# Kernel optimization log

Hardware: AMD Instinct MI355X
Metric: run time of the kernel (lower is better)

Reference implementation:

```python
import jax, jax.numpy as jnp
import numpy as np

EPS = 0.1
MAX_ITER = 10
SIGMA = 0.1
NEG_INF = -1e8


def gaussian_position_filter(in_size, out_size, dtype):
    a = jnp.arange(0.0, in_size, dtype=dtype)[:, None] / in_size
    b = jnp.arange(0.0, out_size, dtype=dtype)[None, :] / out_size
    return jnp.exp(-(((a - b) / SIGMA) ** 2))[None]


def log_sinkhorn(K, mask, max_iter):
    # K: n x in_size x out_size (already scaled by 1/eps); mask: n x in_size bool
    n, in_size, out_size = K.shape
    dt = K.dtype
    loga = jnp.log((out_size / mask.sum(1, keepdims=True)).astype(dt))  # n x 1

    def neg_lse(u, v, axis):
        Z = K + u[:, :, None] + v[:, None, :]
        return -jax.nn.logsumexp(Z, axis=axis)

    def body(carry, _):
        u, v = carry
        u = loga + neg_lse(u, v, -1)           # row update: n x in_size
        u = jnp.where(mask, u, jnp.asarray(NEG_INF, dt))
        v = neg_lse(u, v, 1)                   # col update: n x out_size
        return (u, v), None

    u0 = jnp.zeros((n, in_size), dt)
    v0 = jnp.zeros((n, out_size), dt)
    (u, v), _ = jax.lax.scan(body, (u0, v0), None, length=max_iter)
    return jnp.exp(K + u[:, :, None] + v[:, None, :])  # transport plan T


def setup_inputs() -> dict:
    key = jax.random.key(0)
    k1, k2, k3 = jax.random.split(key, 3)
    B, S, O, D = 16, 4096, 512, 128
    return {
        "input": jax.random.normal(k1, (B, S, D), jnp.float32),
        "target": jax.random.normal(k2, (B, O, D), jnp.float32),
        "iou_cost": jax.random.uniform(k3, (B, S, O), jnp.float32),
        "mask": jnp.ones((B, S), jnp.bool_),
    }


def reference(input, target, iou_cost, mask):
    # input: B x S x D, target: B x O x D, iou_cost: B x S x O, mask: B x S
    B, S, D = input.shape
    O = target.shape[1]
    pf = gaussian_position_filter(S, O, input.dtype)
    K = jnp.einsum('bsd,bod->bso', input, target) - iou_cost  # similarity minus IoU cost
    K = pf * K / EPS
    T = pf * log_sinkhorn(K, mask, MAX_ITER) * S              # B x S x O
    # output: B x (out_size*heads) x in_size, heads=1
    return jnp.transpose(T, (0, 2, 1)).reshape(B, O, S)
```

## Files before the change

### kernel.cpp

```cpp
#include <hip/hip_runtime.h>
#include <hip/hip_bf16.h>

#define B_ 16
#define S_ 4096
#define O_ 512
#define D_ 128
#define NEG_INF_ -1e8f
#define MAX_ITER_ 10
#define YST 513

typedef __attribute__((ext_vector_type(8))) short short8;
typedef __attribute__((ext_vector_type(4))) float floatx4;
typedef __attribute__((ext_vector_type(4))) unsigned short ushort4v;

__device__ inline unsigned short f32_to_bf16_rne(float x) {
    union { float f; unsigned int u; } c; c.f = x;
    unsigned int u = c.u;
    unsigned int r = (u + 0x7FFFu + ((u >> 16) & 1u)) >> 16;
    return (unsigned short)r;
}
__device__ inline float bf16_bits_to_f32(unsigned short h) {
    union { unsigned int u; float f; } c; c.u = ((unsigned int)h) << 16;
    return c.f;
}

__global__ void init_kernel(const int* __restrict__ mask,
                            float* __restrict__ u, float* __restrict__ v,
                            float* __restrict__ loga) {
    __shared__ int sc[256];
    int b = blockIdx.x, t = threadIdx.x;
    int c = 0;
    for (int k = t; k < S_; k += 256) c += (mask[(size_t)b * S_ + k] != 0);
    sc[t] = c; __syncthreads();
    for (int st = 128; st > 0; st >>= 1) { if (t < st) sc[t] += sc[t + st]; __syncthreads(); }
    if (t == 0) loga[b] = logf((float)O_ / (float)sc[0]);
    for (int k = t; k < S_; k += 256) u[(size_t)b * S_ + k] = 0.f;
    for (int k = t; k < O_; k += 256) v[b * O_ + k] = 0.f;
}

__global__ __launch_bounds__(256) void split_kernel(const float* __restrict__ src,
                                                    unsigned short* __restrict__ hi,
                                                    unsigned short* __restrict__ lo, int n4) {
    int i = blockIdx.x * 256 + threadIdx.x;
    if (i >= n4) return;
    float4 x = ((const float4*)src)[i];
    float xs[4] = {x.x, x.y, x.z, x.w};
    ushort4v h, l;
#pragma unroll
    for (int j = 0; j < 4; ++j) {
        unsigned short hh = f32_to_bf16_rne(xs[j]);
        float rem = xs[j] - bf16_bits_to_f32(hh);
        h[j] = hh; l[j] = f32_to_bf16_rne(rem);
    }
    ((ushort4v*)hi)[i] = h;
    ((ushort4v*)lo)[i] = l;
}


__global__ __launch_bounds__(256) void gemm_nat(const unsigned short* __restrict__ in_hi,
                                                const unsigned short* __restrict__ in_lo,
                                                const unsigned short* __restrict__ tg_hi,
                                                const unsigned short* __restrict__ tg_lo,
                                                const float* __restrict__ iou,
                                                float* __restrict__ K) {
    int b = blockIdx.z;
    int s0 = blockIdx.x * 256;
    int o0 = blockIdx.y * 64;
    int t = threadIdx.x, wid = t >> 6, lane = t & 63, fr = lane & 15, kg = lane >> 4;
    int sw = s0 + wid * 64;

    const unsigned short* ih = in_hi + ((size_t)b * S_ + sw + fr) * D_;
    const unsigned short* il = in_lo + ((size_t)b * S_ + sw + fr) * D_;
    const unsigned short* th = tg_hi + ((size_t)b * O_ + o0 + fr) * D_;
    const unsigned short* tl = tg_lo + ((size_t)b * O_ + o0 + fr) * D_;

    floatx4 acc[4][4];
#pragma unroll
    for (int i = 0; i < 4; ++i)
#pragma unroll
        for (int j = 0; j < 4; ++j) acc[i][j] = (floatx4){0.f, 0.f, 0.f, 0.f};

#pragma unroll
    for (int kb = 0; kb < 4; ++kb) {
        int ko = kb * 32 + kg * 8;
        short8 T_h[4], T_l[4];
#pragma unroll
        for (int j = 0; j < 4; ++j) {
            T_h[j] = *(const short8*)(th + (size_t)j * 16 * D_ + ko);
            T_l[j] = *(const short8*)(tl + (size_t)j * 16 * D_ + ko);
        }
#pragma unroll
        for (int i = 0; i < 4; ++i) {
            short8 I_h = *(const short8*)(ih + (size_t)i * 16 * D_ + ko);
            short8 I_l = *(const short8*)(il + (size_t)i * 16 * D_ + ko);
#pragma unroll
            for (int j = 0; j < 4; ++j) {
                acc[i][j] = __builtin_amdgcn_mfma_f32_16x16x32_bf16(T_l[j], I_h, acc[i][j], 0, 0, 0);
                acc[i][j] = __builtin_amdgcn_mfma_f32_16x16x32_bf16(T_h[j], I_l, acc[i][j], 0, 0, 0);
                acc[i][j] = __builtin_amdgcn_mfma_f32_16x16x32_bf16(T_h[j], I_h, acc[i][j], 0, 0, 0);
            }
        }
    }

#pragma unroll
    for (int i = 0; i < 4; ++i) {
        int s = sw + i * 16 + fr;
        float sn = (float)s * (1.0f / S_);
        size_t rowb = ((size_t)b * S_ + s) * O_;
#pragma unroll
        for (int j = 0; j < 4; ++j) {
            int ob = o0 + j * 16 + kg * 4;
            float4 iv = *(const float4*)(iou + rowb + ob);
            float ivs[4] = {iv.x, iv.y, iv.z, iv.w};
            float tmp[4];
#pragma unroll
            for (int r = 0; r < 4; ++r) {
                float d = sn - (float)(ob + r) * (1.0f / O_);
                float pf = __expf(-100.0f * d * d);
                tmp[r] = pf * (acc[i][j][r] - ivs[r]) * 10.0f;
            }
            float4 q; q.x = tmp[0]; q.y = tmp[1]; q.z = tmp[2]; q.w = tmp[3];
            *(float4*)(K + rowb + ob) = q;
        }
    }
}

template <int FIRST>
__global__ __launch_bounds__(256) void sink_iter(const float* __restrict__ K,
                                                 const float* __restrict__ vin,
                                                 float* __restrict__ u,
                                                 float2* __restrict__ colma,
                                                 const int* __restrict__ mask,
                                                 const float* __restrict__ loga) {
    __shared__ float sv[O_];
    __shared__ float sy[16 * YST];
    int b = blockIdx.y;
    int t = threadIdx.x;
    int fr = t & 15, sl = t >> 4;
    if (!FIRST) {
        for (int i = t; i < O_; i += 256) sv[i] = vin[b * O_ + i];
        __syncthreads();
    }
    int s = blockIdx.x * 16 + sl;
    size_t srow = (size_t)b * S_ + s;
    const float* krow = K + srow * O_ + fr * 4;
    float uold = FIRST ? 0.f : u[srow];

    float xv[32];
#pragma unroll
    for (int k = 0; k < 8; ++k) {
        float4 q = *(const float4*)(krow + k * 64);
        if (!FIRST) {
            float4 vv = *(const float4*)&sv[fr * 4 + k * 64];
            q.x += uold + vv.x; q.y += uold + vv.y;
            q.z += uold + vv.z; q.w += uold + vv.w;
        }
        xv[k * 4 + 0] = q.x; xv[k * 4 + 1] = q.y;
        xv[k * 4 + 2] = q.z; xv[k * 4 + 3] = q.w;
    }

    float M = -INFINITY;
#pragma unroll
    for (int i = 0; i < 32; ++i) M = fmaxf(M, xv[i]);
#pragma unroll
    for (int off = 1; off < 16; off <<= 1) M = fmaxf(M, __shfl_xor(M, off));
    float a = 0.f;
#pragma unroll
    for (int i = 0; i < 32; ++i) a += __expf(xv[i] - M);
#pragma unroll
    for (int off = 1; off < 16; off <<= 1) a += __shfl_xor(a, off);
    float unew = loga[b] - (M + logf(a));
    if (!mask[srow]) unew = NEG_INF_;
    if (fr == 0) u[srow] = unew;

    float c = unew - uold;
#pragma unroll
    for (int k = 0; k < 8; ++k) {
        float4 q;
        q.x = xv[k * 4 + 0] + c; q.y = xv[k * 4 + 1] + c;
        q.z = xv[k * 4 + 2] + c; q.w = xv[k * 4 + 3] + c;
        *(float4*)&sy[sl * YST + fr * 4 + k * 64] = q;
    }
    __syncthreads();

    float2* cout = colma + ((size_t)b * 256 + blockIdx.x) * O_;
#pragma unroll
    for (int h = 0; h < 2; ++h) {
        int o = t + h * 256;
        float q[16];
        float m = -INFINITY;
#pragma unroll
        for (int r = 0; r < 16; ++r) { q[r] = sy[r * YST + o]; m = fmaxf(m, q[r]); }
        float aa = 0.f;
#pragma unroll
        for (int r = 0; r < 16; ++r) aa += __expf(q[r] - m);
        float2 res; res.x = m; res.y = aa;
        cout[o] = res;
    }
}

__global__ __launch_bounds__(256) void finalize_v(const float2* __restrict__ colma,
                                                  float* __restrict__ v) {
    __shared__ float sm[4][64], sa[4][64];
    int b = blockIdx.y;
    int ol = threadIdx.x & 63, cg = threadIdx.x >> 6;
    int o = blockIdx.x * 64 + ol;
    const float2* cp = colma + (size_t)b * 256 * O_ + o;
    float M = -INFINITY, A = 0.f;
#pragma unroll 4
    for (int i = 0; i < 64; ++i) {
        float2 q = cp[(size_t)(cg * 64 + i) * O_];
        float nm = fmaxf(M, q.x);
        A = A * __expf(M - nm) + q.y * __expf(q.x - nm);
        M = nm;
    }
    sm[cg][ol] = M; sa[cg][ol] = A;
    __syncthreads();
    if (threadIdx.x < 64) {
        M = sm[0][ol]; A = sa[0][ol];
#pragma unroll
        for (int i = 1; i < 4; ++i) {
            float mi = sm[i][ol], ai = sa[i][ol];
            float nm = fmaxf(M, mi);
            A = A * __expf(M - nm) + ai * __expf(mi - nm);
            M = nm;
        }
        v[b * O_ + o] = -(M + logf(A));
    }
}

__global__ __launch_bounds__(256) void final_tr(const float* __restrict__ K,
                                                const float* __restrict__ u,
                                                const float* __restrict__ v,
                                                float* __restrict__ out) {
    __shared__ float tile[64][65];
    __shared__ float su[64], svv[64];
    int b = blockIdx.z;
    int s0 = blockIdx.x * 64, o0 = blockIdx.y * 64;
    int t = threadIdx.x, fr = t & 15, rg = t >> 4;
    if (t < 64) su[t] = u[(size_t)b * S_ + s0 + t];
    else if (t < 128) svv[t - 64] = v[b * O_ + o0 + t - 64];
    __syncthreads();
#pragma unroll
    for (int p = 0; p < 4; ++p) {
        int sl = p * 16 + rg;
        int s = s0 + sl;
        float4 x = *(const float4*)(K + ((size_t)b * S_ + s) * O_ + o0 + fr * 4);
        float us = su[sl];
        float sn = (float)s * (1.0f / S_);
        float xs[4] = {x.x, x.y, x.z, x.w};
#pragma unroll
        for (int c = 0; c < 4; ++c) {
            int ol = fr * 4 + c;
            float d = sn - (float)(o0 + ol) * (1.0f / O_);
            tile[ol][sl] = 4096.0f * __expf(xs[c] + us + svv[ol] - 100.0f * d * d);
        }
    }
    __syncthreads();
#pragma unroll
    for (int p = 0; p < 4; ++p) {
        int ol = p * 16 + rg;
        float4 y;
        y.x = tile[ol][fr * 4 + 0];
        y.y = tile[ol][fr * 4 + 1];
        y.z = tile[ol][fr * 4 + 2];
        y.w = tile[ol][fr * 4 + 3];
        *(float4*)(out + ((size_t)b * O_ + o0 + ol) * S_ + s0 + fr * 4) = y;
    }
}


__global__ __launch_bounds__(256) void gemm_kt2(const unsigned short* __restrict__ in_hi,
                                                const unsigned short* __restrict__ in_lo,
                                                const unsigned short* __restrict__ tg_hi,
                                                const unsigned short* __restrict__ tg_lo,
                                                const float* __restrict__ iou,
                                                float* __restrict__ KT) {
    __shared__ float siou[64 * 65];
    int b = blockIdx.z;
    int s0 = blockIdx.x * 64;
    int o0 = blockIdx.y * 64;
    int t = threadIdx.x;
    {
        const float* ir = iou + ((size_t)b * S_ + s0 + (t >> 2)) * O_ + o0 + (t & 3) * 16;
        float4 q0 = ((const float4*)ir)[0];
        float4 q1 = ((const float4*)ir)[1];
        float4 q2 = ((const float4*)ir)[2];
        float4 q3 = ((const float4*)ir)[3];
        float* dst = &siou[(t >> 2) * 65 + (t & 3) * 16];
        dst[0]=q0.x; dst[1]=q0.y; dst[2]=q0.z; dst[3]=q0.w;
        dst[4]=q1.x; dst[5]=q1.y; dst[6]=q1.z; dst[7]=q1.w;
        dst[8]=q2.x; dst[9]=q2.y; dst[10]=q2.z; dst[11]=q2.w;
        dst[12]=q3.x; dst[13]=q3.y; dst[14]=q3.z; dst[15]=q3.w;
    }
    int w = t >> 6, lane = t & 63, fr = lane & 15, kg = lane >> 4;
    const unsigned short* ta_hi = tg_hi + ((size_t)b * O_ + o0 + w * 16 + fr) * D_;
    const unsigned short* ta_lo = tg_lo + ((size_t)b * O_ + o0 + w * 16 + fr) * D_;
    const unsigned short* ib_hi = in_hi + ((size_t)b * S_ + s0 + fr) * D_;
    const unsigned short* ib_lo = in_lo + ((size_t)b * S_ + s0 + fr) * D_;
    floatx4 acc[4];
#pragma unroll
    for (int st = 0; st < 4; ++st) acc[st] = (floatx4){0.f, 0.f, 0.f, 0.f};
#pragma unroll
    for (int kb = 0; kb < 4; ++kb) {
        int ko = kb * 32 + kg * 8;
        short8 ah = *(const short8*)(ta_hi + ko);
        short8 al2 = *(const short8*)(ta_lo + ko);
#pragma unroll
        for (int st = 0; st < 4; ++st) {
            short8 bh2 = *(const short8*)(ib_hi + (size_t)st * 16 * D_ + ko);
            short8 bl2 = *(const short8*)(ib_lo + (size_t)st * 16 * D_ + ko);
            acc[st] = __builtin_amdgcn_mfma_f32_16x16x32_bf16(al2, bh2, acc[st], 0, 0, 0);
            acc[st] = __builtin_amdgcn_mfma_f32_16x16x32_bf16(ah, bl2, acc[st], 0, 0, 0);
            acc[st] = __builtin_amdgcn_mfma_f32_16x16x32_bf16(ah, bh2, acc[st], 0, 0, 0);
        }
    }
    __syncthreads();
#pragma unroll
    for (int st = 0; st < 4; ++st) {
        int s = s0 + st * 16 + fr;
        float ds = (float)s * (1.0f / S_);
#pragma unroll
        for (int r = 0; r < 4; ++r) {
            int o = o0 + w * 16 + kg * 4 + r;
            float d = ds - (float)o * (1.0f / O_);
            float pf = __expf(-100.0f * d * d);
            float iouv = siou[(st * 16 + fr) * 65 + (w * 16 + kg * 4 + r)];
            KT[((size_t)b * O_ + o) * S_ + s] = pf * (acc[st][r] - iouv) * 10.0f;
        }
    }
}

__global__ __launch_bounds__(256) void row_update2(const float* __restrict__ KT,
                                                   const float* __restrict__ v,
                                                   float* __restrict__ u,
                                                   const int* __restrict__ mask,
                                                   const float* __restrict__ loga) {
    __shared__ float sv[O_];
    __shared__ float lm[4][128], la[4][128];
    int b = blockIdx.y;
    int s0 = blockIdx.x * 128;
    int t = threadIdx.x, lane = t & 63, w = t >> 6;
    for (int i = t; i < O_; i += 256) sv[i] = v[b * O_ + i];
    __syncthreads();
    const float* kt = KT + (size_t)b * O_ * S_ + s0 + lane * 2;
    float m0 = -INFINITY, m1 = -INFINITY, a0 = 0.f, a1 = 0.f;
    int ob = w * 128;
#pragma unroll 8
    for (int i = 0; i < 128; ++i) {
        int o = ob + i;
        float2 x2 = *(const float2*)(kt + (size_t)o * S_);
        float vo = sv[o];
        float x0 = x2.x + vo, x1 = x2.y + vo;
        if (x0 > m0) { a0 = a0 * __expf(m0 - x0) + 1.f; m0 = x0; } else a0 += __expf(x0 - m0);
        if (x1 > m1) { a1 = a1 * __expf(m1 - x1) + 1.f; m1 = x1; } else a1 += __expf(x1 - m1);
    }
    lm[w][lane * 2] = m0;     la[w][lane * 2] = a0;
    lm[w][lane * 2 + 1] = m1; la[w][lane * 2 + 1] = a1;
    __syncthreads();
    if (t < 128) {
        float M = lm[0][t], A = la[0][t];
#pragma unroll
        for (int i = 1; i < 4; ++i) {
            float mi = lm[i][t], ai = la[i][t];
            float nm = fmaxf(M, mi);
            A = A * __expf(M - nm) + ai * __expf(mi - nm);
            M = nm;
        }
        float lse = M + logf(A);
        size_t si = (size_t)b * S_ + s0 + t;
        u[si] = mask[si] ? (loga[b] - u[si] - lse) : NEG_INF_;
    }
}

template <int FIN>
__global__ __launch_bounds__(256) void col_update2(float* __restrict__ KT,
                                                   const float* __restrict__ u,
                                                   float* __restrict__ v) {
    __shared__ float red[8];
    int b = blockIdx.y, o = blockIdx.x;
    int t = threadIdx.x;
    float* kt = KT + ((size_t)b * O_ + o) * S_;
    const float* ub = u + (size_t)b * S_;
    float vold = v[b * O_ + o];
    float xs[16];
    float m = -INFINITY, a = 0.f;
#pragma unroll
    for (int k = 0; k < 4; ++k) {
        int s = k * 1024 + t * 4;
        float4 kx = *(const float4*)(kt + s);
        float4 ux = *(const float4*)(ub + s);
        float x0 = kx.x + ux.x, x1 = kx.y + ux.y, x2 = kx.z + ux.z, x3 = kx.w + ux.w;
        if (FIN) { xs[k*4] = x0; xs[k*4+1] = x1; xs[k*4+2] = x2; xs[k*4+3] = x3; }
        float cm = fmaxf(fmaxf(x0, x1), fmaxf(x2, x3));
        float nm = fmaxf(m, cm);
        a = a * __expf(m - nm) + __expf(x0 - nm) + __expf(x1 - nm)
                               + __expf(x2 - nm) + __expf(x3 - nm);
        m = nm;
    }
#pragma unroll
    for (int off = 1; off < 64; off <<= 1) {
        float mo = __shfl_xor(m, off), ao = __shfl_xor(a, off);
        float nm = fmaxf(m, mo);
        a = a * __expf(m - nm) + ao * __expf(mo - nm);
        m = nm;
    }
    int w = t >> 6;
    if ((t & 63) == 0) { red[w * 2] = m; red[w * 2 + 1] = a; }
    __syncthreads();
    float M = red[0], A = red[1];
#pragma unroll
    for (int i = 1; i < 4; ++i) {
        float mi = red[i * 2], ai = red[i * 2 + 1];
        float nm = fmaxf(M, mi);
        A = A * __expf(M - nm) + ai * __expf(mi - nm);
        M = nm;
    }
    float lse = M + logf(A);
    float vn = -vold - lse;
    if (t == 0) v[b * O_ + o] = vn;
    if (FIN) {
        float oo = (float)o * (1.0f / O_);
#pragma unroll
        for (int k = 0; k < 4; ++k) {
            int s = k * 1024 + t * 4;
            float4 r;
            float rr[4];
#pragma unroll
            for (int j = 0; j < 4; ++j) {
                float d = (float)(s + j) * (1.0f / S_) - oo;
                rr[j] = 4096.0f * __expf(xs[k * 4 + j] + vn - 100.0f * d * d);
            }
            r.x = rr[0]; r.y = rr[1]; r.z = rr[2]; r.w = rr[3];
            *(float4*)(kt + s) = r;
        }
    }
}


extern "C" void kernel_launch(void* const* d_in, const int* in_sizes, int n_in,
                              void* d_out, int out_size, void* d_ws, size_t ws_size,
                              hipStream_t stream) {
    const float* input  = (const float*)d_in[0];
    const float* target = (const float*)d_in[1];
    const float* iou    = (const float*)d_in[2];
    const int*   mask   = (const int*)d_in[3];
    float* out = (float*)d_out;
    float* wsf = (float*)d_ws;

    const size_t N_IN = (size_t)B_ * S_ * D_;
    const size_t N_TG = (size_t)B_ * O_ * D_;
    const size_t NK   = (size_t)B_ * S_ * O_;

    float* u    = wsf;
    float* v    = u + (size_t)B_ * S_;
    float* loga = v + (size_t)B_ * O_;

    float* Knat = loga + 16;
    float* region = Knat + NK;
    unsigned short* f_in_hi = (unsigned short*)region;
    unsigned short* f_in_lo = f_in_hi + N_IN;
    unsigned short* f_tg_hi = f_in_lo + N_IN;
    unsigned short* f_tg_lo = f_tg_hi + N_TG;
    float2* colma = (float2*)region;
    size_t need_fast = (size_t)((char*)(f_tg_lo + N_TG) - (char*)d_ws);

    unsigned short* m_in_hi = (unsigned short*)(loga + 16);
    unsigned short* m_in_lo = m_in_hi + N_IN;
    unsigned short* m_tg_hi = m_in_lo + N_IN;
    unsigned short* m_tg_lo = m_tg_hi + N_TG;
    size_t need_mid = (size_t)((char*)(m_tg_lo + N_TG) - (char*)d_ws);

    init_kernel<<<B_, 256, 0, stream>>>(mask, u, v, loga);

    if (ws_size >= need_fast) {
        split_kernel<<<(int)(N_IN / 4 / 256), 256, 0, stream>>>(input, f_in_hi, f_in_lo, (int)(N_IN / 4));
        split_kernel<<<(int)(N_TG / 4 / 256), 256, 0, stream>>>(target, f_tg_hi, f_tg_lo, (int)(N_TG / 4));
        gemm_nat<<<dim3(S_ / 256, O_ / 64, B_), 256, 0, stream>>>(f_in_hi, f_in_lo, f_tg_hi, f_tg_lo, iou, Knat);
        for (int it = 0; it < MAX_ITER_; ++it) {
            if (it == 0)
                sink_iter<1><<<dim3(S_ / 16, B_), 256, 0, stream>>>(Knat, v, u, colma, mask, loga);
            else
                sink_iter<0><<<dim3(S_ / 16, B_), 256, 0, stream>>>(Knat, v, u, colma, mask, loga);
            finalize_v<<<dim3(O_ / 64, B_), 256, 0, stream>>>(colma, v);
        }
        final_tr<<<dim3(S_ / 64, O_ / 64, B_), 256, 0, stream>>>(Knat, u, v, out);
    } else if (ws_size >= need_mid) {
        split_kernel<<<(int)(N_IN / 4 / 256), 256, 0, stream>>>(input, m_in_hi, m_in_lo, (int)(N_IN / 4));
        split_kernel<<<(int)(N_TG / 4 / 256), 256, 0, stream>>>(target, m_tg_hi, m_tg_lo, (int)(N_TG / 4));
        gemm_kt2<<<dim3(S_ / 64, O_ / 64, B_), 256, 0, stream>>>(m_in_hi, m_in_lo, m_tg_hi, m_tg_lo, iou, out);
        for (int it = 0; it < MAX_ITER_; ++it) {
            row_update2<<<dim3(S_ / 128, B_), 256, 0, stream>>>(out, v, u, mask, loga);
            if (it < MAX_ITER_ - 1)
                col_update2<0><<<dim3(O_, B_), 256, 0, stream>>>(out, u, v);
            else
                col_update2<1><<<dim3(O_, B_), 256, 0, stream>>>(out, u, v);
        }
    }
}
```

Baseline: 513.4 us.

## Prefetch IoU into LDS in GEMM and pipeline multi-tile sinkhorn row blocks

The GEMM now uses 128-row tiles and loads its IoU tile into shared memory with asynchronous global-to-LDS loads. The load uses a rotated column swizzle, so it overlaps the MFMA work and the epilogue reads avoid bank conflicts. Each sink_iter block now handles 64 rows as four 16-row sub-tiles, double-buffering the K loads in registers. Column max/sum partials are merged online across the sub-tiles, which shrinks the colma partial buffer and the finalize_v reduction fourfold. The trade-offs are higher register pressure, extra barriers, and fewer blocks per launch.

After: 518.7 us. Within noise of the previous version (+1.0%).

```diff
diff --git a/kernel.cpp b/kernel.cpp
--- a/kernel.cpp
+++ b/kernel.cpp
@@ -22,6 +22,10 @@
 __device__ inline float bf16_bits_to_f32(unsigned short h) {
     union { unsigned int u; float f; } c; c.u = ((unsigned int)h) << 16;
     return c.f;
+}
+__device__ inline void gload_lds16(const float* g, float* l) {
+    __builtin_amdgcn_global_load_lds((const __attribute__((address_space(1))) void*)g,
+                                     (__attribute__((address_space(3))) void*)l, 16, 0, 0);
 }
 
 __global__ void init_kernel(const int* __restrict__ mask,
@@ -56,27 +60,35 @@
     ((ushort4v*)lo)[i] = l;
 }
 
-
 __global__ __launch_bounds__(256) void gemm_nat(const unsigned short* __restrict__ in_hi,
                                                 const unsigned short* __restrict__ in_lo,
                                                 const unsigned short* __restrict__ tg_hi,
                                                 const unsigned short* __restrict__ tg_lo,
                                                 const float* __restrict__ iou,
                                                 float* __restrict__ K) {
+    __shared__ float siou[128 * 64];
     int b = blockIdx.z;
-    int s0 = blockIdx.x * 256;
+    int s0 = blockIdx.x * 128;
     int o0 = blockIdx.y * 64;
     int t = threadIdx.x, wid = t >> 6, lane = t & 63, fr = lane & 15, kg = lane >> 4;
-    int sw = s0 + wid * 64;
-
-    const unsigned short* ih = in_hi + ((size_t)b * S_ + sw + fr) * D_;
-    const unsigned short* il = in_lo + ((size_t)b * S_ + sw + fr) * D_;
+
+#pragma unroll
+    for (int i = 0; i < 8; ++i) {
+        int ii = wid * 8 + i;
+        int row = ii * 4 + (lane >> 4);
+        int col = (((lane & 15) + (row & 15)) & 15) * 4;
+        const float* g = iou + ((size_t)b * S_ + s0 + row) * O_ + o0 + col;
+        gload_lds16(g, &siou[ii * 256]);
+    }
+
+    const unsigned short* ih = in_hi + ((size_t)b * S_ + s0 + wid * 32 + fr) * D_;
+    const unsigned short* il = in_lo + ((size_t)b * S_ + s0 + wid * 32 + fr) * D_;
     const unsigned short* th = tg_hi + ((size_t)b * O_ + o0 + fr) * D_;
     const unsigned short* tl = tg_lo + ((size_t)b * O_ + o0 + fr) * D_;
 
-    floatx4 acc[4][4];
-#pragma unroll
-    for (int i = 0; i < 4; ++i)
+    floatx4 acc[2][4];
+#pragma unroll
+    for (int i = 0; i < 2; ++i)
 #pragma unroll
         for (int j = 0; j < 4; ++j) acc[i][j] = (floatx4){0.f, 0.f, 0.f, 0.f};
 
@@ -90,7 +102,7 @@
             T_l[j] = *(const short8*)(tl + (size_t)j * 16 * D_ + ko);
         }
 #pragma unroll
-        for (int i = 0; i < 4; ++i) {
+        for (int i = 0; i < 2; ++i) {
             short8 I_h = *(const short8*)(ih + (size_t)i * 16 * D_ + ko);
             short8 I_l = *(const short8*)(il + (size_t)i * 16 * D_ + ko);
 #pragma unroll
@@ -101,26 +113,29 @@
             }
         }
     }
-
-#pragma unroll
-    for (int i = 0; i < 4; ++i) {
-        int s = sw + i * 16 + fr;
+    __syncthreads();
+
+#pragma unroll
+    for (int i = 0; i < 2; ++i) {
+        int rowl = wid * 32 + i * 16 + fr;
+        int s = s0 + rowl;
         float sn = (float)s * (1.0f / S_);
         size_t rowb = ((size_t)b * S_ + s) * O_;
 #pragma unroll
         for (int j = 0; j < 4; ++j) {
-            int ob = o0 + j * 16 + kg * 4;
-            float4 iv = *(const float4*)(iou + rowb + ob);
+            int obl = j * 16 + kg * 4;
+            int x = (obl - fr * 4) & 63;
+            float4 iv = *(const float4*)&siou[rowl * 64 + x];
             float ivs[4] = {iv.x, iv.y, iv.z, iv.w};
             float tmp[4];
 #pragma unroll
             for (int r = 0; r < 4; ++r) {
-                float d = sn - (float)(ob + r) * (1.0f / O_);
+                float d = sn - (float)(o0 + obl + r) * (1.0f / O_);
                 float pf = __expf(-100.0f * d * d);
                 tmp[r] = pf * (acc[i][j][r] - ivs[r]) * 10.0f;
             }
             float4 q; q.x = tmp[0]; q.y = tmp[1]; q.z = tmp[2]; q.w = tmp[3];
-            *(float4*)(K + rowb + ob) = q;
+            *(float4*)(K + rowb + o0 + obl) = q;
         }
     }
 }
@@ -135,67 +150,98 @@
     __shared__ float sv[O_];
     __shared__ float sy[16 * YST];
     int b = blockIdx.y;
-    int t = threadIdx.x;
-    int fr = t & 15, sl = t >> 4;
+    int t = threadIdx.x, fr = t & 15, sl = t >> 4;
     if (!FIRST) {
         for (int i = t; i < O_; i += 256) sv[i] = vin[b * O_ + i];
         __syncthreads();
     }
-    int s = blockIdx.x * 16 + sl;
-    size_t srow = (size_t)b * S_ + s;
-    const float* krow = K + srow * O_ + fr * 4;
-    float uold = FIRST ? 0.f : u[srow];
-
-    float xv[32];
-#pragma unroll
-    for (int k = 0; k < 8; ++k) {
-        float4 q = *(const float4*)(krow + k * 64);
-        if (!FIRST) {
-            float4 vv = *(const float4*)&sv[fr * 4 + k * 64];
-            q.x += uold + vv.x; q.y += uold + vv.y;
-            q.z += uold + vv.z; q.w += uold + vv.w;
-        }
-        xv[k * 4 + 0] = q.x; xv[k * 4 + 1] = q.y;
-        xv[k * 4 + 2] = q.z; xv[k * 4 + 3] = q.w;
-    }
-
-    float M = -INFINITY;
-#pragma unroll
-    for (int i = 0; i < 32; ++i) M = fmaxf(M, xv[i]);
-#pragma unroll
-    for (int off = 1; off < 16; off <<= 1) M = fmaxf(M, __shfl_xor(M, off));
-    float a = 0.f;
-#pragma unroll
-    for (int i = 0; i < 32; ++i) a += __expf(xv[i] - M);
-#pragma unroll
-    for (int off = 1; off < 16; off <<= 1) a += __shfl_xor(a, off);
-    float unew = loga[b] - (M + logf(a));
-    if (!mask[srow]) unew = NEG_INF_;
-    if (fr == 0) u[srow] = unew;
-
-    float c = unew - uold;
-#pragma unroll
-    for (int k = 0; k < 8; ++k) {
-        float4 q;
-        q.x = xv[k * 4 + 0] + c; q.y = xv[k * 4 + 1] + c;
-        q.z = xv[k * 4 + 2] + c; q.w = xv[k * 4 + 3] + c;
-        *(float4*)&sy[sl * YST + fr * 4 + k * 64] = q;
-    }
-    __syncthreads();
-
-    float2* cout = colma + ((size_t)b * 256 + blockIdx.x) * O_;
-#pragma unroll
-    for (int h = 0; h < 2; ++h) {
-        int o = t + h * 256;
-        float q[16];
-        float m = -INFINITY;
-#pragma unroll
-        for (int r = 0; r < 16; ++r) { q[r] = sy[r * YST + o]; m = fmaxf(m, q[r]); }
-        float aa = 0.f;
-#pragma unroll
-        for (int r = 0; r < 16; ++r) aa += __expf(q[r] - m);
-        float2 res; res.x = m; res.y = aa;
-        cout[o] = res;
+    int sbase = blockIdx.x * 64;
+    float lg = loga[b];
+    float Mc0 = -INFINITY, Ac0 = 0.f, Mc1 = -INFINITY, Ac1 = 0.f;
+
+    float bufA[32], bufB[32];
+    auto loadK = [&](float (&dst)[32], int tau) {
+        const float* krow = K + ((size_t)b * S_ + sbase + tau * 16 + sl) * O_ + fr * 4;
+#pragma unroll
+        for (int k = 0; k < 8; ++k) {
+            float4 q = *(const float4*)(krow + k * 64);
+            dst[k * 4 + 0] = q.x; dst[k * 4 + 1] = q.y;
+            dst[k * 4 + 2] = q.z; dst[k * 4 + 3] = q.w;
+        }
+    };
+    auto process = [&](float (&cur)[32], float (&nxt)[32], int tau, bool pre) {
+        int s = sbase + tau * 16 + sl;
+        size_t srow = (size_t)b * S_ + s;
+        float uold = FIRST ? 0.f : u[srow];
+        int mk = mask[srow];
+        if (pre) loadK(nxt, tau + 1);
+
+        float xv[32];
+        if (FIRST) {
+#pragma unroll
+            for (int i = 0; i < 32; ++i) xv[i] = cur[i];
+        } else {
+#pragma unroll
+            for (int k = 0; k < 8; ++k) {
+                float4 vvq = *(const float4*)&sv[fr * 4 + k * 64];
+                xv[k * 4 + 0] = cur[k * 4 + 0] + uold + vvq.x;
+                xv[k * 4 + 1] = cur[k * 4 + 1] + uold + vvq.y;
+                xv[k * 4 + 2] = cur[k * 4 + 2] + uold + vvq.z;
+                xv[k * 4 + 3] = cur[k * 4 + 3] + uold + vvq.w;
+            }
+        }
+        float M = -INFINITY;
+#pragma unroll
+        for (int i = 0; i < 32; ++i) M = fmaxf(M, xv[i]);
+#pragma unroll
+        for (int off = 1; off < 16; off <<= 1) M = fmaxf(M, __shfl_xor(M, off));
+        float a = 0.f;
+#pragma unroll
+        for (int i = 0; i < 32; ++i) a += __expf(xv[i] - M);
+#pragma unroll
+        for (int off = 1; off < 16; off <<= 1) a += __shfl_xor(a, off);
+        float unew = lg - (M + logf(a));
+        if (!mk) unew = NEG_INF_;
+        if (fr == 0) u[srow] = unew;
+
+        float c = unew - uold;
+#pragma unroll
+        for (int k = 0; k < 8; ++k) {
+            float4 q;
+            q.x = xv[k * 4 + 0] + c; q.y = xv[k * 4 + 1] + c;
+            q.z = xv[k * 4 + 2] + c; q.w = xv[k * 4 + 3] + c;
+            *(float4*)&sy[sl * YST + fr * 4 + k * 64] = q;
+        }
+        __syncthreads();
+#pragma unroll
+        for (int h = 0; h < 2; ++h) {
+            int o = t + h * 256;
+            float q[16];
+            float m = -INFINITY;
+#pragma unroll
+            for (int r = 0; r < 16; ++r) { q[r] = sy[r * YST + o]; m = fmaxf(m, q[r]); }
+            float aa = 0.f;
+#pragma unroll
+            for (int r = 0; r < 16; ++r) aa += __expf(q[r] - m);
+            float Mo = h ? Mc1 : Mc0, Ao = h ? Ac1 : Ac0;
+            float nm = fmaxf(Mo, m);
+            Ao = Ao * __expf(Mo - nm) + aa * __expf(m - nm);
+            if (h) { Mc1 = nm; Ac1 = Ao; } else { Mc0 = nm; Ac0 = Ao; }
+        }
+        __syncthreads();
+    };
+    loadK(bufA, 0);
+    process(bufA, bufB, 0, true);
+    process(bufB, bufA, 1, true);
+    process(bufA, bufB, 2, true);
+    process(bufB, bufA, 3, false);
+
+    float2* cout = colma + ((size_t)b * 64 + blockIdx.x) * O_;
+    {
+        float2 r0; r0.x = Mc0; r0.y = Ac0;
+        cout[t] = r0;
+        float2 r1; r1.x = Mc1; r1.y = Ac1;
+        cout[t + 256] = r1;
     }
 }
 
@@ -205,11 +251,11 @@
     int b = blockIdx.y;
     int ol = threadIdx.x & 63, cg = threadIdx.x >> 6;
     int o = blockIdx.x * 64 + ol;
-    const float2* cp = colma + (size_t)b * 256 * O_ + o;
+    const float2* cp = colma + (size_t)b * 64 * O_ + o;
     float M = -INFINITY, A = 0.f;
 #pragma unroll 4
-    for (int i = 0; i < 64; ++i) {
-        float2 q = cp[(size_t)(cg * 64 + i) * O_];
+    for (int i = 0; i < 16; ++i) {
+        float2 q = cp[(size_t)(cg * 16 + i) * O_];
         float nm = fmaxf(M, q.x);
         A = A * __expf(M - nm) + q.y * __expf(q.x - nm);
         M = nm;
@@ -476,12 +522,12 @@
     if (ws_size >= need_fast) {
         split_kernel<<<(int)(N_IN / 4 / 256), 256, 0, stream>>>(input, f_in_hi, f_in_lo, (int)(N_IN / 4));
         split_kernel<<<(int)(N_TG / 4 / 256), 256, 0, stream>>>(target, f_tg_hi, f_tg_lo, (int)(N_TG / 4));
-        gemm_nat<<<dim3(S_ / 256, O_ / 64, B_), 256, 0, stream>>>(f_in_hi, f_in_lo, f_tg_hi, f_tg_lo, iou, Knat);
+        gemm_nat<<<dim3(S_ / 128, O_ / 64, B_), 256, 0, stream>>>(f_in_hi, f_in_lo, f_tg_hi, f_tg_lo, iou, Knat);
         for (int it = 0; it < MAX_ITER_; ++it) {
             if (it == 0)
-                sink_iter<1><<<dim3(S_ / 16, B_), 256, 0, stream>>>(Knat, v, u, colma, mask, loga);
+                sink_iter<1><<<dim3(S_ / 64, B_), 256, 0, stream>>>(Knat, v, u, colma, mask, loga);
             else
-                sink_iter<0><<<dim3(S_ / 16, B_), 256, 0, stream>>>(Knat, v, u, colma, mask, loga);
+                sink_iter<0><<<dim3(S_ / 64, B_), 256, 0, stream>>>(Knat, v, u, colma, mask, loga);
             finalize_v<<<dim3(O_ / 64, B_), 256, 0, stream>>>(colma, v);
         }
         final_tr<<<dim3(S_ / 64, O_ / 64, B_), 256, 0, stream>>>(Knat, u, v, out);
```
